# Kernel optimization log

Measured on AMD Instinct MI355X. Metric: run time of the kernel, lower is better.

The kernel has to match this reference:

```python
import jax, jax.numpy as jnp
import numpy as np

B, L, D = 16, 512, 512
T_MAX = 4096  # mel_max_length: static pad target (upper bound on sum of durations)


def setup_inputs() -> dict:
    key = jax.random.key(0)
    kx, kd = jax.random.split(key)
    x = jax.random.normal(kx, (B, L, D), dtype=jnp.float32)
    duration_tokens = jax.random.randint(kd, (B, L), 0, 8, dtype=jnp.int32)
    return {"x": x, "duration_tokens": duration_tokens, "mel_max_length": T_MAX}


def reference(x, duration_tokens, mel_max_length):
    # LengthRegulator: out[b, t] = x[b, j] where token j covers output frame t,
    # i.e. the alignment matmul  alignment @ x  expressed as cumsum + searchsorted + gather.
    b, l, d = x.shape
    ends = jnp.cumsum(duration_tokens, axis=1)            # [B, L] exclusive frame ends
    t = jnp.arange(mel_max_length, dtype=ends.dtype)      # [T]
    # token index covering each frame t: first j with ends[j] > t
    tok = jax.vmap(lambda e: jnp.searchsorted(e, t, side='right'))(ends)  # [B, T]
    valid = t[None, :] < ends[:, -1:]                     # frames beyond total duration -> zero pad
    tok = jnp.clip(tok, 0, l - 1)
    out = jnp.take_along_axis(x, tok[:, :, None], axis=1)  # [B, T, D]
    return jnp.where(valid[:, :, None], out, jnp.zeros((), dtype=x.dtype))
```

## Files before the change

### kernel.cpp

```cpp
#include <hip/hip_runtime.h>


#define BATCH 16
#define LTOK  512
#define DIM   512
#define TMAX  4096

__global__ __launch_bounds__(LTOK) void MRTE_cumsum_kernel(const int* __restrict__ dur,
                                                           int* __restrict__ ends) {
    __shared__ int s[LTOK];
    const int b   = blockIdx.x;
    const int tid = threadIdx.x;
    s[tid] = dur[b * LTOK + tid];
    __syncthreads();
    #pragma unroll
    for (int off = 1; off < LTOK; off <<= 1) {
        int v = (tid >= off) ? s[tid - off] : 0;
        __syncthreads();
        s[tid] += v;
        __syncthreads();
    }
    ends[b * LTOK + tid] = s[tid];
}

__global__ __launch_bounds__(128) void MRTE_gather_kernel(const float* __restrict__ x,
                                                          const int* __restrict__ ends,
                                                          float* __restrict__ out) {
    const int t   = blockIdx.x;
    const int b   = blockIdx.y;
    const int tid = threadIdx.x;

    const int* __restrict__ e = ends + b * LTOK;
    const int total = e[LTOK - 1];

    float4* __restrict__ orow =
        reinterpret_cast<float4*>(out + ((size_t)b * TMAX + (size_t)t) * DIM);

    if (t >= total) {
        orow[tid] = make_float4(0.f, 0.f, 0.f, 0.f);
        return;
    }

    int lo = 0, hi = LTOK;
    while (lo < hi) {
        int mid = (lo + hi) >> 1;
        if (e[mid] > t) hi = mid; else lo = mid + 1;
    }

    const float4* __restrict__ xrow =
        reinterpret_cast<const float4*>(x + ((size_t)b * LTOK + (size_t)lo) * DIM);
    orow[tid] = xrow[tid];
}

extern "C" void kernel_launch(void* const* d_in, const int* in_sizes, int n_in,
                              void* d_out, int out_size, void* d_ws, size_t ws_size,
                              hipStream_t stream) {
    const float* x   = (const float*)d_in[0];
    const int*   dur = (const int*)d_in[1];
    float* out = (float*)d_out;
    int*   ends = (int*)d_ws;

    MRTE_cumsum_kernel<<<BATCH, LTOK, 0, stream>>>(dur, ends);
    MRTE_gather_kernel<<<dim3(TMAX, BATCH), 128, 0, stream>>>(x, ends, out);
}
```

Baseline: 160.2 us.

## Batch gather rows per block with shared ends, linear token walk and nontemporal stores

The gather kernel now handles eight output frames per 256-thread block. It stages the batch's cumulative ends in LDS, does one binary search per block, and advances the token index linearly for each later row. Output rows are written with nontemporal stores. The cumsum kernel is replaced by a wavefront shuffle scan plus a cross-wave add. This cuts per-row global binary-search latency and launch granularity, but each thread now does a serial loop over rows.

```diff
diff --git a/kernel.cpp b/kernel.cpp
--- a/kernel.cpp
+++ b/kernel.cpp
@@ -5,51 +5,71 @@
 #define LTOK  512
 #define DIM   512
 #define TMAX  4096
+#define ROWS  8
 
-__global__ __launch_bounds__(LTOK) void MRTE_cumsum_kernel(const int* __restrict__ dur,
-                                                           int* __restrict__ ends) {
-    __shared__ int s[LTOK];
-    const int b   = blockIdx.x;
-    const int tid = threadIdx.x;
-    s[tid] = dur[b * LTOK + tid];
+typedef float nt_f4 __attribute__((ext_vector_type(4)));
+
+__global__ __launch_bounds__(512) void MRTE_cumsum_kernel(const int* __restrict__ dur,
+                                                          int* __restrict__ ends) {
+    const int b    = blockIdx.x;
+    const int tid  = threadIdx.x;
+    const int lane = tid & 63;
+    const int wid  = tid >> 6;
+    __shared__ int wsum[8];
+
+    int v = dur[b * LTOK + tid];
+    #pragma unroll
+    for (int off = 1; off < 64; off <<= 1) {
+        int n = __shfl_up(v, off, 64);
+        if (lane >= off) v += n;
+    }
+    if (lane == 63) wsum[wid] = v;
     __syncthreads();
+    int add = 0;
     #pragma unroll
-    for (int off = 1; off < LTOK; off <<= 1) {
-        int v = (tid >= off) ? s[tid - off] : 0;
-        __syncthreads();
-        s[tid] += v;
-        __syncthreads();
-    }
-    ends[b * LTOK + tid] = s[tid];
+    for (int w = 0; w < 7; ++w)
+        add += (w < wid) ? wsum[w] : 0;
+    ends[b * LTOK + tid] = v + add;
 }
 
-__global__ __launch_bounds__(128) void MRTE_gather_kernel(const float* __restrict__ x,
+__global__ __launch_bounds__(256) void MRTE_gather_kernel(const float* __restrict__ x,
                                                           const int* __restrict__ ends,
                                                           float* __restrict__ out) {
-    const int t   = blockIdx.x;
-    const int b   = blockIdx.y;
-    const int tid = threadIdx.x;
+    __shared__ int se[LTOK];
+    const int b    = blockIdx.y;
+    const int t0   = blockIdx.x * ROWS;
+    const int tid  = threadIdx.x;
+    const int half = tid >> 7;
+    const int lane = tid & 127;
 
-    const int* __restrict__ e = ends + b * LTOK;
-    const int total = e[LTOK - 1];
+    se[tid]       = ends[b * LTOK + tid];
+    se[tid + 256] = ends[b * LTOK + tid + 256];
+    __syncthreads();
 
-    float4* __restrict__ orow =
-        reinterpret_cast<float4*>(out + ((size_t)b * TMAX + (size_t)t) * DIM);
-
-    if (t >= total) {
-        orow[tid] = make_float4(0.f, 0.f, 0.f, 0.f);
-        return;
-    }
+    const int total = se[LTOK - 1];
 
     int lo = 0, hi = LTOK;
     while (lo < hi) {
         int mid = (lo + hi) >> 1;
-        if (e[mid] > t) hi = mid; else lo = mid + 1;
+        if (se[mid] > t0) hi = mid; else lo = mid + 1;
     }
 
-    const float4* __restrict__ xrow =
-        reinterpret_cast<const float4*>(x + ((size_t)b * LTOK + (size_t)lo) * DIM);
-    orow[tid] = xrow[tid];
+    const nt_f4* __restrict__ xb =
+        reinterpret_cast<const nt_f4*>(x + (size_t)b * LTOK * DIM);
+    nt_f4* __restrict__ ob =
+        reinterpret_cast<nt_f4*>(out + ((size_t)b * TMAX + (size_t)t0) * DIM);
+
+    int jt = lo;
+    #pragma unroll
+    for (int r = 0; r < ROWS; r += 2) {
+        const int t = t0 + r + half;
+        nt_f4 v = (nt_f4)0.f;
+        if (t < total) {
+            while (se[jt] <= t) ++jt;
+            v = xb[(size_t)jt * (DIM / 4) + lane];
+        }
+        __builtin_nontemporal_store(v, &ob[(size_t)(r + half) * (DIM / 4) + lane]);
+    }
 }
 
 extern "C" void kernel_launch(void* const* d_in, const int* in_sizes, int n_in,
@@ -57,9 +77,9 @@
                               hipStream_t stream) {
     const float* x   = (const float*)d_in[0];
     const int*   dur = (const int*)d_in[1];
-    float* out = (float*)d_out;
+    float* out  = (float*)d_out;
     int*   ends = (int*)d_ws;
 
     MRTE_cumsum_kernel<<<BATCH, LTOK, 0, stream>>>(dur, ends);
-    MRTE_gather_kernel<<<dim3(TMAX, BATCH), 128, 0, stream>>>(x, ends, out);
+    MRTE_gather_kernel<<<dim3(TMAX / ROWS, BATCH), 256, 0, stream>>>(x, ends, out);
 }
```

Measured after the change: 159.3 us. No clear change (-0.6%).
